# Optimization experiments

Measured on AMD Instinct MI355X. Metric: run time of the kernel, lower is better.

Reference implementation:

```python
import jax, jax.numpy as jnp
import numpy as np

BATCH = 4
STATE_LEN = 8
SEQ_LEN = 4080          # middle tokens; total = SEQ_LEN + 2*STATE_LEN = 4096 (multiple of 8 -> no pad branch)
DIM_IN = 512
DIM_K = 64
DIM_V = 64
SCALE = 0.125           # 1/sqrt(DIM_K)
TOTAL = SEQ_LEN + 2 * STATE_LEN


def setup_inputs() -> dict:
    key = jax.random.key(0)
    ks = jax.random.split(key, 7)
    sd = 1.0 / np.sqrt(DIM_IN)  # ~ nn.Linear init scale
    x = jax.random.normal(ks[0], (BATCH, TOTAL, DIM_IN), dtype=jnp.float32)
    # weights stored as (in, out): y = x @ W  (equivalent to torch Linear with W.T)
    Wq = jax.random.normal(ks[1], (DIM_IN, DIM_K), dtype=jnp.float32) * sd
    Wk = jax.random.normal(ks[2], (DIM_IN, DIM_K), dtype=jnp.float32) * sd
    Wv = jax.random.normal(ks[3], (DIM_IN, DIM_V), dtype=jnp.float32) * sd
    Wq_s = jax.random.normal(ks[4], (DIM_IN, DIM_K), dtype=jnp.float32) * sd
    Wk_s = jax.random.normal(ks[5], (DIM_IN, DIM_K), dtype=jnp.float32) * sd
    Wv_s = jax.random.normal(ks[6], (DIM_IN, DIM_V), dtype=jnp.float32) * sd
    return {"x": x, "Wq": Wq, "Wk": Wk, "Wv": Wv, "Wq_s": Wq_s, "Wk_s": Wk_s, "Wv_s": Wv_s}


def reference(x, Wq, Wk, Wv, Wq_s, Wk_s, Wv_s):
    # extract_state: [state_start | middle | state_end]
    x_ss = x[:, :STATE_LEN]
    x_mid = x[:, STATE_LEN:STATE_LEN + SEQ_LEN]
    x_se = x[:, STATE_LEN + SEQ_LEN:]
    # state tokens use the *_state projections; middle tokens the normal ones
    q = jnp.concatenate([x_ss @ Wq_s, x_mid @ Wq, x_se @ Wq_s], axis=1).astype(jnp.float32)
    k = jnp.concatenate([x_ss @ Wk_s, x_mid @ Wk, x_se @ Wk_s], axis=1).astype(jnp.float32)
    v = jnp.concatenate([x_ss @ Wv_s, x_mid @ Wv, x_se @ Wv_s], axis=1).astype(jnp.float32)
    T = q.shape[1]  # TOTAL
    # scores: (B, T, T); causal mask = log(tril(ones)) == 0 / -inf
    scores = jnp.einsum('bqd,bkd->bqk', q, k) * SCALE
    causal = jnp.tril(jnp.ones((T, T), dtype=bool))
    scores = jnp.where(causal[None], scores, -jnp.inf)
    att = jax.nn.softmax(scores, axis=-1)
    out = jnp.einsum('bqk,bkv->bqv', att, v)
    return out.astype(x.dtype)
```

## Files before the change

kernel.cpp:

```cpp
#include <hip/hip_runtime.h>
#include <hip/hip_bf16.h>

typedef unsigned short u16;
typedef __attribute__((ext_vector_type(8))) short short8;
typedef __attribute__((ext_vector_type(16))) float f32x16;

#define MFMA(A,B,C) __builtin_amdgcn_mfma_f32_32x32x16_bf16(A,B,C,0,0,0)
#define NEG_INF -1e30f

__device__ __forceinline__ unsigned cvtpk_bf16(float a, float b) {
    unsigned r;
    asm("v_cvt_pk_bf16_f32 %0, %1, %2" : "=v"(r) : "v"(a), "v"(b));
    return r;
}
__device__ __forceinline__ void permswap(unsigned &a, unsigned &b) {
    auto r = __builtin_amdgcn_permlane32_swap(a, b, false, false);
    a = r[0]; b = r[1];
}
union W4u { unsigned u[4]; short8 v; };
__device__ __forceinline__ short8 mk8(unsigned a, unsigned b, unsigned c, unsigned d) {
    W4u w; w.u[0] = a; w.u[1] = b; w.u[2] = c; w.u[3] = d; return w.v;
}
__device__ __forceinline__ void split_words(float p0, float p1, unsigned &wh, unsigned &wl) {
    wh = cvtpk_bf16(p0, p1);
    float h0 = __uint_as_float(wh << 16);
    float h1 = __uint_as_float(wh & 0xffff0000u);
    wl = cvtpk_bf16(p0 - h0, p1 - h1);
}
__device__ __forceinline__ void split_store(float v, u16* ph, u16* pl) {
    __hip_bfloat16 h = __float2bfloat16(v);
    float hf = __bfloat162float(h);
    __hip_bfloat16 l = __float2bfloat16(v - hf);
    *ph = *(u16*)&h;
    *pl = *(u16*)&l;
}
__device__ __forceinline__ short8 ld8(const u16* p) { return *(const short8*)p; }

__device__ __forceinline__ int cb64(int qs, int lc) {
    int u = qs >> lc, r = qs - (u << lc);
    return (((u * (u + 1)) >> 1) << lc) + r * (u + 1);
}

__device__ __forceinline__ size_t qk_idx(int grow, int col) {
    return (size_t)(grow >> 5) * 2048 + (col >> 4) * 512 + (grow & 31) * 16
         + ((col >> 3) & 1) * 8 + (col & 7);
}

__device__ __forceinline__ void pack_strip(const f32x16 &ca, const f32x16 &cb,
                                           short8 *pbh, short8 *pbl) {
    unsigned wAh, wAl, wBh, wBl, wCh, wCl, wDh, wDl;
    split_words(ca[0], ca[1], wAh, wAl);   split_words(ca[2], ca[3], wBh, wBl);
    split_words(ca[4], ca[5], wCh, wCl);   split_words(ca[6], ca[7], wDh, wDl);
    permswap(wAh, wCh); permswap(wBh, wDh); permswap(wAl, wCl); permswap(wBl, wDl);
    pbh[0] = mk8(wAh, wBh, wCh, wDh); pbl[0] = mk8(wAl, wBl, wCl, wDl);
    split_words(ca[8], ca[9], wAh, wAl);   split_words(ca[10], ca[11], wBh, wBl);
    split_words(ca[12], ca[13], wCh, wCl); split_words(ca[14], ca[15], wDh, wDl);
    permswap(wAh, wCh); permswap(wBh, wDh); permswap(wAl, wCl); permswap(wBl, wDl);
    pbh[1] = mk8(wAh, wBh, wCh, wDh); pbl[1] = mk8(wAl, wBl, wCl, wDl);
    split_words(cb[0], cb[1], wAh, wAl);   split_words(cb[2], cb[3], wBh, wBl);
    split_words(cb[4], cb[5], wCh, wCl);   split_words(cb[6], cb[7], wDh, wDl);
    permswap(wAh, wCh); permswap(wBh, wDh); permswap(wAl, wCl); permswap(wBl, wDl);
    pbh[2] = mk8(wAh, wBh, wCh, wDh); pbl[2] = mk8(wAl, wBl, wCl, wDl);
    split_words(cb[8], cb[9], wAh, wAl);   split_words(cb[10], cb[11], wBh, wBl);
    split_words(cb[12], cb[13], wCh, wCl); split_words(cb[14], cb[15], wDh, wDl);
    permswap(wAh, wCh); permswap(wBh, wDh); permswap(wAl, wCl); permswap(wBl, wDl);
    pbh[3] = mk8(wAh, wBh, wCh, wDh); pbl[3] = mk8(wAl, wBl, wCl, wDl);
}

__global__ void convw_kernel(
    const float* __restrict__ Wq, const float* __restrict__ Wk, const float* __restrict__ Wv,
    const float* __restrict__ Wqs, const float* __restrict__ Wks, const float* __restrict__ Wvs,
    u16* __restrict__ wbase)
{
    const int z = blockIdx.y;
    const int tile = blockIdx.x;
    const float* W = (z == 0) ? Wq : (z == 1) ? Wk : (z == 2) ? Wv
                   : (z == 3) ? Wqs : (z == 4) ? Wks : Wvs;
    u16* oh = wbase + (size_t)z * 65536;
    u16* ol = oh + 32768;
    __shared__ float Xs[64][65];
    __shared__ u16 stg[8192];
    const int tid = threadIdx.x;
    const int d0 = tile * 64;
    #pragma unroll
    for (int k = 0; k < 16; ++k) {
        int idx = tid + k * 256;
        int d = idx >> 6, c = idx & 63;
        Xs[d][c] = W[(size_t)(d0 + d) * 64 + c];
    }
    __syncthreads();
    #pragma unroll
    for (int k = 0; k < 16; ++k) {
        int odx = tid + k * 256;
        int j = odx & 7, hi8 = (odx >> 3) & 1, r = (odx >> 4) & 63, sl = odx >> 10;
        split_store(Xs[sl * 16 + hi8 * 8 + j][r], &stg[odx], &stg[4096 + odx]);
    }
    __syncthreads();
    #pragma unroll
    for (int rep = 0; rep < 2; ++rep) {
        int i = (tid * 2 + rep) * 8;
        *(short8*)&oh[(size_t)tile * 4096 + i] = *(const short8*)&stg[i];
        *(short8*)&ol[(size_t)tile * 4096 + i] = *(const short8*)&stg[4096 + i];
    }
}

__global__ __launch_bounds__(128, 2) void proj_kernel(
    const float* __restrict__ x, const u16* __restrict__ wbase,
    u16* __restrict__ qh, u16* __restrict__ ql,
    u16* __restrict__ kh, u16* __restrict__ kl,
    u16* __restrict__ vth, u16* __restrict__ vtl)
{
    __shared__ __align__(16) char smraw[24576];
    float (*red)[16][64] = (float (*)[16][64])smraw;
    u16* stg = (u16*)smraw;

    const int bid = blockIdx.x;
    const bool edge = (bid >= 512);
    int sidx;
    if (!edge) { int xcd = bid & 7; sidx = (xcd >> 1) * 128 + (xcd & 1) * 64 + (bid >> 3); }
    else sidx = bid;
    const int w = threadIdx.x >> 6;
    const int lane = threadIdx.x & 63;
    const int l31 = lane & 31, hi = lane >> 5;

    const u16* wb = wbase + (edge ? (size_t)3 * 65536 : 0);
    const u16* wqh_ = wb;                 const u16* wql_ = wb + 32768;
    const u16* wkh_ = wb + 65536;         const u16* wkl_ = wb + 65536 + 32768;
    const u16* wvh_ = wb + 2 * 65536;     const u16* wvl_ = wb + 2 * 65536 + 32768;

    int growA;
    if (!edge) growA = sidx * 32 + l31;
    else {
        int e = sidx - 512, rb = l31 >> 4, i = l31 & 15;
        growA = (2 * e + rb) * 4096 + (i < 8 ? i : 4080 + i);
    }
    const float* xrow = x + (size_t)growA * 512;

    f32x16 aq[2] = {{}, {}}, ak[2] = {{}, {}}, av[2] = {{}, {}};
    const int s0 = w * 16;
    #pragma unroll 2
    for (int si = 0; si < 16; ++si) {
        const int s = s0 + si;
        const int d0 = s * 16 + 8 * hi;
        float4 xa = *(const float4*)(xrow + d0);
        float4 xb = *(const float4*)(xrow + d0 + 4);
        unsigned xh_[4], xl_[4];
        split_words(xa.x, xa.y, xh_[0], xl_[0]);
        split_words(xa.z, xa.w, xh_[1], xl_[1]);
        split_words(xb.x, xb.y, xh_[2], xl_[2]);
        split_words(xb.z, xb.w, xh_[3], xl_[3]);
        short8 xhf = mk8(xh_[0], xh_[1], xh_[2], xh_[3]);
        short8 xlf = mk8(xl_[0], xl_[1], xl_[2], xl_[3]);
        #pragma unroll
        for (int half = 0; half < 2; ++half) {
            size_t wof = (size_t)s * 1024 + (half * 32 + l31) * 16 + hi * 8;
            short8 qH = ld8(wqh_ + wof), qL = ld8(wql_ + wof);
            short8 kH = ld8(wkh_ + wof), kL = ld8(wkl_ + wof);
            short8 vH = ld8(wvh_ + wof), vL = ld8(wvl_ + wof);
            aq[half] = MFMA(xhf, qH, aq[half]);
            aq[half] = MFMA(xhf, qL, aq[half]);
            aq[half] = MFMA(xlf, qH, aq[half]);
            ak[half] = MFMA(xhf, kH, ak[half]);
            ak[half] = MFMA(xhf, kL, ak[half]);
            ak[half] = MFMA(xlf, kH, ak[half]);
            av[half] = MFMA(vH, xhf, av[half]);
            av[half] = MFMA(vL, xhf, av[half]);
            av[half] = MFMA(vH, xlf, av[half]);
        }
    }
    if (w == 1) {
        #pragma unroll
        for (int h = 0; h < 2; ++h)
            #pragma unroll
            for (int r = 0; r < 16; ++r) {
                red[h][r][lane] = aq[h][r];
                red[2 + h][r][lane] = ak[h][r];
            }
    } else {
        #pragma unroll
        for (int h = 0; h < 2; ++h)
            #pragma unroll
            for (int r = 0; r < 16; ++r) red[4 + h][r][lane] = av[h][r];
    }
    __syncthreads();
    if (w == 0) {
        #pragma unroll
        for (int h = 0; h < 2; ++h)
            #pragma unroll
            for (int r = 0; r < 16; ++r) {
                aq[h][r] += red[h][r][lane];
                ak[h][r] += red[2 + h][r][lane];
            }
    } else {
        #pragma unroll
        for (int h = 0; h < 2; ++h)
            #pragma unroll
            for (int r = 0; r < 16; ++r) av[h][r] += red[4 + h][r][lane];
    }
    __syncthreads();

    if (!edge) {
        if (w == 0) {
            #pragma unroll
            for (int half = 0; half < 2; ++half)
                #pragma unroll
                for (int r = 0; r < 16; ++r) {
                    const int crow = (r & 3) + 8 * (r >> 2) + 4 * hi;
                    const int col = half * 32 + l31;
                    int loff = (col >> 4) * 512 + crow * 16 + ((col >> 3) & 1) * 8 + (col & 7);
                    split_store(aq[half][r] * 0.125f, &stg[loff], &stg[2048 + loff]);
                    split_store(ak[half][r], &stg[4096 + loff], &stg[6144 + loff]);
                }
        } else {
            #pragma unroll
            for (int half = 0; half < 2; ++half)
                #pragma unroll
                for (int r = 0; r < 16; ++r) {
                    const int crow = (r & 3) + 8 * (r >> 2) + 4 * hi;
                    int lv = half * 1024 + (l31 >> 4) * 512 + crow * 16
                           + ((l31 >> 3) & 1) * 8 + (l31 & 7);
                    split_store(av[half][r], &stg[8192 + lv], &stg[10240 + lv]);
                }
        }
        __syncthreads();
        const int t128 = threadIdx.x;
        const int sloc = sidx & 127;
        u16* qk0 = qh + (size_t)sidx * 2048;
        u16* qk1 = ql + (size_t)sidx * 2048;
        u16* qk2 = kh + (size_t)sidx * 2048;
        u16* qk3 = kl + (size_t)sidx * 2048;
        #pragma unroll
        for (int rep = 0; rep < 2; ++rep) {
            int i = (t128 * 2 + rep) * 8;
            int crow_ = (i >> 4) & 31;
            int tin = sloc * 32 + crow_;
            if (tin >= 8 && tin < 4088) {
                *(short8*)&qk0[i] = *(const short8*)&stg[i];
                *(short8*)&qk1[i] = *(const short8*)&stg[2048 + i];
                *(short8*)&qk2[i] = *(const short8*)&stg[4096 + i];
                *(short8*)&qk3[i] = *(const short8*)&stg[6144 + i];
            }
        }
        const size_t Vbase = (size_t)(sidx >> 1) * 4096;
        #pragma unroll
        for (int rep = 0; rep < 2; ++rep) {
            int i = (t128 * 2 + rep) * 8;
            int T = ((i >> 9) & 1) * 16 + ((i >> 3) & 1) * 8;
            int tbase = sloc * 32 + T;
            if (tbase >= 8 && tbase < 4088) {
                size_t go = Vbase + (size_t)(i >> 10) * 2048
                          + (((sidx & 1) << 1) + ((i >> 9) & 1)) * 512 + (i & 511);
                *(short8*)&vth[go] = *(const short8*)&stg[8192 + i];
                *(short8*)&vtl[go] = *(const short8*)&stg[10240 + i];
            }
        }
    } else {
        const int bv = growA >> 12, tv = growA & 4095;
        if (w == 0) {
            #pragma unroll
            for (int half = 0; half < 2; ++half)
                #pragma unroll
                for (int r = 0; r < 16; ++r) {
                    const int crow = (r & 3) + 8 * (r >> 2) + 4 * hi;
                    const int col = half * 32 + l31;
                    int e = sidx - 512, rb = crow >> 4, i = crow & 15;
                    int growC = (2 * e + rb) * 4096 + (i < 8 ? i : 4080 + i);
                    size_t qo = qk_idx(growC, col);
                    split_store(aq[half][r] * 0.125f, qh + qo, ql + qo);
                    split_store(ak[half][r], kh + qo, kl + qo);
                }
        } else {
            #pragma unroll
            for (int half = 0; half < 2; ++half)
                #pragma unroll
                for (int r = 0; r < 16; ++r) {
                    const int crow = (r & 3) + 8 * (r >> 2) + 4 * hi;
                    size_t vo = (size_t)(bv * 64 + (tv >> 6)) * 4096 + half * 2048
                              + ((tv & 63) >> 4) * 512 + crow * 16
                              + ((tv >> 3) & 1) * 8 + (tv & 7);
                    split_store(av[half][r], vth + vo, vtl + vo);
                }
        }
    }
}

__global__ __launch_bounds__(64, 2) void flash_kernel(
    const u16* __restrict__ qhB, const u16* __restrict__ qlB,
    const u16* __restrict__ khB, const u16* __restrict__ klB,
    const u16* __restrict__ vthB, const u16* __restrict__ vtlB,
    float* __restrict__ Opart, float* __restrict__ mpart, float* __restrict__ lpart,
    int lc, int G)
{
    const int bid = blockIdx.x;
    const int xcd = bid & 7;
    const int b = xcd >> 1, par = xcd & 1;
    const int rr = bid >> 3;
    const int chunk = (G - 1) - (2 * rr + par);
    int qs = 0;
    for (int step = 32; step; step >>= 1) {
        int cand = qs + step;
        if (cand < 64 && cb64(cand, lc) <= chunk) qs = cand;
    }
    const int cloc = chunk - cb64(qs, lc);
    const int nt = qs + 1;
    const int klo = cloc << lc;
    const int lim = klo + (1 << lc);
    const int khi = (nt < lim) ? nt : lim;
    const int lane = threadIdx.x, l31 = lane & 31, hi = lane >> 5;
    const size_t lane_off = (size_t)(l31 * 16 + hi * 8);

    const size_t qb0 = (size_t)(b * 128 + qs * 2) * 2048 + lane_off;
    short8 q0h[4], q0l[4], q1h[4], q1l[4];
    #pragma unroll
    for (int s = 0; s < 4; ++s) {
        q0h[s] = ld8(qhB + qb0 + s * 512);
        q0l[s] = ld8(qlB + qb0 + s * 512);
        q1h[s] = ld8(qhB + qb0 + 2048 + s * 512);
        q1l[s] = ld8(qlB + qb0 + 2048 + s * 512);
    }

    f32x16 o00 = {}, o01 = {}, o10 = {}, o11 = {};
    float m0 = NEG_INF, l0 = 0.f, m1 = NEG_INF, l1 = 0.f;

    for (int kb = klo; kb < khi; ++kb) {
        const bool diag = (kb == qs);
        const size_t kt = (size_t)(b * 128 + kb * 2) * 2048 + lane_off;
        short8 kf[4];
        f32x16 c00 = {}, c01 = {}, c11 = {};
        f32x16 c10;
        #pragma unroll
        for (int r = 0; r < 16; ++r) c10[r] = diag ? NEG_INF : 0.f;

        #pragma unroll
        for (int s = 0; s < 4; ++s) kf[s] = ld8(khB + kt + s * 512);
        __builtin_amdgcn_s_setprio(1);
        #pragma unroll
        for (int s = 0; s < 4; ++s) {
            c00 = MFMA(kf[s], q0h[s], c00);
            c00 = MFMA(kf[s], q0l[s], c00);
            c01 = MFMA(kf[s], q1h[s], c01);
            c01 = MFMA(kf[s], q1l[s], c01);
        }
        __builtin_amdgcn_s_setprio(0);
        #pragma unroll
        for (int s = 0; s < 4; ++s) kf[s] = ld8(klB + kt + s * 512);
        __builtin_amdgcn_s_setprio(1);
        #pragma unroll
        for (int s = 0; s < 4; ++s) {
            c00 = MFMA(kf[s], q0h[s], c00);
            c01 = MFMA(kf[s], q1h[s], c01);
        }
        __builtin_amdgcn_s_setprio(0);
        #pragma unroll
        for (int s = 0; s < 4; ++s) kf[s] = ld8(khB + kt + 2048 + s * 512);
        __builtin_amdgcn_s_setprio(1);
        if (!diag) {
            #pragma unroll
            for (int s = 0; s < 4; ++s) {
                c10 = MFMA(kf[s], q0h[s], c10);
                c10 = MFMA(kf[s], q0l[s], c10);
            }
        }
        #pragma unroll
        for (int s = 0; s < 4; ++s) {
            c11 = MFMA(kf[s], q1h[s], c11);
            c11 = MFMA(kf[s], q1l[s], c11);
        }
        __builtin_amdgcn_s_setprio(0);
        #pragma unroll
        for (int s = 0; s < 4; ++s) kf[s] = ld8(klB + kt + 2048 + s * 512);
        __builtin_amdgcn_s_setprio(1);
        if (!diag) {
            #pragma unroll
            for (int s = 0; s < 4; ++s) c10 = MFMA(kf[s], q0h[s], c10);
        }
        #pragma unroll
        for (int s = 0; s < 4; ++s) c11 = MFMA(kf[s], q1h[s], c11);
        __builtin_amdgcn_s_setprio(0);

        if (diag) {
            #pragma unroll
            for (int r = 0; r < 16; ++r) {
                int krow = (r & 3) + 8 * (r >> 2) + 4 * hi;
                if (krow > l31) { c00[r] = NEG_INF; c11[r] = NEG_INF; }
            }
        }
        float mx0 = NEG_INF, mx1 = NEG_INF;
        #pragma unroll
        for (int r = 0; r < 16; ++r) {
            mx0 = fmaxf(mx0, fmaxf(c00[r], c10[r]));
            mx1 = fmaxf(mx1, fmaxf(c01[r], c11[r]));
        }
        mx0 = fmaxf(mx0, __shfl_xor(mx0, 32));
        mx1 = fmaxf(mx1, __shfl_xor(mx1, 32));
        float mn0 = fmaxf(m0, mx0), mn1 = fmaxf(m1, mx1);
        float al0 = __expf(m0 - mn0), al1 = __expf(m1 - mn1);
        m0 = mn0; m1 = mn1;
        float s0 = 0.f, s1 = 0.f;
        #pragma unroll
        for (int r = 0; r < 16; ++r) {
            c00[r] = __expf(c00[r] - mn0); s0 += c00[r];
            c10[r] = __expf(c10[r] - mn0); s0 += c10[r];
            c01[r] = __expf(c01[r] - mn1); s1 += c01[r];
            c11[r] = __expf(c11[r] - mn1); s1 += c11[r];
        }
        s0 += __shfl_xor(s0, 32);
        s1 += __shfl_xor(s1, 32);
        l0 = l0 * al0 + s0;
        l1 = l1 * al1 + s1;
        #pragma unroll
        for (int r = 0; r < 16; ++r) {
            o00[r] *= al0; o10[r] *= al0;
            o01[r] *= al1; o11[r] *= al1;
        }
        short8 p0h[4], p0l[4], p1h[4], p1l[4];
        pack_strip(c00, c10, p0h, p0l);
        pack_strip(c01, c11, p1h, p1l);

        __builtin_amdgcn_sched_barrier(0);
        const size_t vt = (size_t)(b * 64 + kb) * 4096 + lane_off;
        short8 vh_[4], vl_[4];
        #pragma unroll
        for (int s = 0; s < 4; ++s) {
            vh_[s] = ld8(vthB + vt + s * 512);
            vl_[s] = ld8(vtlB + vt + s * 512);
        }
        __builtin_amdgcn_s_setprio(1);
        #pragma unroll
        for (int s = 0; s < 4; ++s) {
            o00 = MFMA(vh_[s], p0h[s], o00);
            o00 = MFMA(vh_[s], p0l[s], o00);
            o00 = MFMA(vl_[s], p0h[s], o00);
            o01 = MFMA(vh_[s], p1h[s], o01);
            o01 = MFMA(vh_[s], p1l[s], o01);
            o01 = MFMA(vl_[s], p1h[s], o01);
        }
        __builtin_amdgcn_s_setprio(0);
        #pragma unroll
        for (int s = 0; s < 4; ++s) {
            vh_[s] = ld8(vthB + vt + 2048 + s * 512);
            vl_[s] = ld8(vtlB + vt + 2048 + s * 512);
        }
        __builtin_amdgcn_s_setprio(1);
        #pragma unroll
        for (int s = 0; s < 4; ++s) {
            o10 = MFMA(vh_[s], p0h[s], o10);
            o10 = MFMA(vh_[s], p0l[s], o10);
            o10 = MFMA(vl_[s], p0h[s], o10);
            o11 = MFMA(vh_[s], p1h[s], o11);
            o11 = MFMA(vh_[s], p1l[s], o11);
            o11 = MFMA(vl_[s], p1h[s], o11);
        }
        __builtin_amdgcn_s_setprio(0);
    }
    const int pid = b * G + chunk;
    float* Op = Opart + (size_t)pid * 4096;
    #pragma unroll
    for (int r = 0; r < 16; ++r) {
        int v0 = (r & 3) + 8 * (r >> 2) + 4 * hi;
        Op[v0 * 64 + l31]        = o00[r];
        Op[v0 * 64 + 32 + l31]   = o01[r];
        Op[(v0 + 32) * 64 + l31]      = o10[r];
        Op[(v0 + 32) * 64 + 32 + l31] = o11[r];
    }
    if (hi == 0) {
        mpart[pid * 64 + l31] = m0;       lpart[pid * 64 + l31] = l0;
        mpart[pid * 64 + 32 + l31] = m1;  lpart[pid * 64 + 32 + l31] = l1;
    }
}

__global__ void merge_kernel(
    const float* __restrict__ Opart, const float* __restrict__ mpart,
    const float* __restrict__ lpart, float* __restrict__ out, int lc, int G)
{
    __shared__ float wgt[32][64];
    __shared__ float tr[64][65];
    const int bid = blockIdx.x;
    const int b = bid >> 6, qs = bid & 63;
    const int g = (qs + (1 << lc)) >> lc;
    const int base = b * G + cb64(qs, lc);
    const int tid = threadIdx.x;
    if (tid < 64) {
        float M = NEG_INF;
        for (int s = 0; s < g; ++s) M = fmaxf(M, mpart[(base + s) * 64 + tid]);
        float L = 0.f;
        for (int s = 0; s < g; ++s)
            L += lpart[(base + s) * 64 + tid] * __expf(mpart[(base + s) * 64 + tid] - M);
        float inv = 1.0f / L;
        for (int s = 0; s < g; ++s)
            wgt[s][tid] = __expf(mpart[(base + s) * 64 + tid] - M) * inv;
    }
    __syncthreads();
    float acc[16] = {};
    for (int s = 0; s < g; ++s) {
        const float* Op = Opart + (size_t)(base + s) * 4096;
        #pragma unroll
        for (int k = 0; k < 16; ++k) {
            int i = tid + k * 256;
            acc[k] += wgt[s][i & 63] * Op[i];
        }
    }
    #pragma unroll
    for (int k = 0; k < 16; ++k) {
        int i = tid + k * 256;
        tr[i & 63][i >> 6] = acc[k];
    }
    __syncthreads();
    float* dst = out + ((size_t)b * 4096 + qs * 64) * 64;
    #pragma unroll
    for (int k = 0; k < 16; ++k) {
        int j = tid + k * 256;
        dst[j] = tr[j >> 6][j & 63];
    }
}

extern "C" void kernel_launch(void* const* d_in, const int* in_sizes, int n_in,
                              void* d_out, int out_size, void* d_ws, size_t ws_size,
                              hipStream_t stream) {
    const float* x   = (const float*)d_in[0];
    const float* Wq  = (const float*)d_in[1];
    const float* Wk  = (const float*)d_in[2];
    const float* Wv  = (const float*)d_in[3];
    const float* Wqs = (const float*)d_in[4];
    const float* Wks = (const float*)d_in[5];
    const float* Wvs = (const float*)d_in[6];
    float* out = (float*)d_out;

    char* ws = (char*)d_ws;
    const size_t MB = 1024 * 1024;
    u16* qh  = (u16*)(ws);
    u16* ql  = (u16*)(ws + 2 * MB);
    u16* kh  = (u16*)(ws + 4 * MB);
    u16* kl  = (u16*)(ws + 6 * MB);
    u16* vth = (u16*)(ws + 8 * MB);
    u16* vtl = (u16*)(ws + 10 * MB);
    u16* wbase = (u16*)(ws + 12 * MB);
    float* mpart = (float*)(ws + 13 * MB);
    float* lpart = (float*)(ws + 14 * MB + 512 * 1024);
    float* Opart = (float*)(ws + 16 * MB);

    int LC = 1, G = 1056;
    if (ws_size < 16 * MB + (size_t)4 * 1056 * 16384) { LC = 2; G = 544; }
    if (ws_size < 16 * MB + (size_t)4 * 544  * 16384) { LC = 3; G = 288; }

    convw_kernel<<<dim3(8, 6), 256, 0, stream>>>(Wq, Wk, Wv, Wqs, Wks, Wvs, wbase);
    proj_kernel<<<514, 128, 0, stream>>>(x, wbase, qh, ql, kh, kl, vth, vtl);
    flash_kernel<<<4 * G, 64, 0, stream>>>(qh, ql, kh, kl, vth, vtl,
                                           Opart, mpart, lpart, LC, G);
    merge_kernel<<<256, 256, 0, stream>>>(Opart, mpart, lpart, out, LC, G);
}
```

Baseline: 174.2 us.

## Drop low-bf16 halves of K and V, use exp2 with folded log2e scale

K and V are now stored only as single bf16 (high part), while Q keeps its hi/lo split. This removes the kl/vtl workspace buffers and their loads, and cuts the QK MFMA count from 6 to 4 per strip and the PV count from 3 to 2 per accumulator. The softmax scale now includes log2(e), so a raw v_exp_f32 (exp2) replaces __expf in the flash and merge kernels. The K and V loads are hoisted ahead of the MFMA blocks, and the default split count changes from LC=1 to LC=2. Dropping the K/V low halves lowers accuracy, roughly to bf16 precision on K and V.

```diff
diff --git a/kernel.cpp b/kernel.cpp
--- a/kernel.cpp
+++ b/kernel.cpp
@@ -7,7 +7,13 @@
 
 #define MFMA(A,B,C) __builtin_amdgcn_mfma_f32_32x32x16_bf16(A,B,C,0,0,0)
 #define NEG_INF -1e30f
-
+#define QSC (0.125f * 1.44269504f)
+
+__device__ __forceinline__ float exp2_fast(float x) {
+    float r;
+    asm("v_exp_f32 %0, %1" : "=v"(r) : "v"(x));
+    return r;
+}
 __device__ __forceinline__ unsigned cvtpk_bf16(float a, float b) {
     unsigned r;
     asm("v_cvt_pk_bf16_f32 %0, %1, %2" : "=v"(r) : "v"(a), "v"(b));
@@ -33,6 +39,10 @@
     __hip_bfloat16 l = __float2bfloat16(v - hf);
     *ph = *(u16*)&h;
     *pl = *(u16*)&l;
+}
+__device__ __forceinline__ void store_hi(float v, u16* ph) {
+    __hip_bfloat16 h = __float2bfloat16(v);
+    *ph = *(u16*)&h;
 }
 __device__ __forceinline__ short8 ld8(const u16* p) { return *(const short8*)p; }
 
@@ -107,8 +117,7 @@
 __global__ __launch_bounds__(128, 2) void proj_kernel(
     const float* __restrict__ x, const u16* __restrict__ wbase,
     u16* __restrict__ qh, u16* __restrict__ ql,
-    u16* __restrict__ kh, u16* __restrict__ kl,
-    u16* __restrict__ vth, u16* __restrict__ vtl)
+    u16* __restrict__ kh, u16* __restrict__ vth)
 {
     __shared__ __align__(16) char smraw[24576];
     float (*red)[16][64] = (float (*)[16][64])smraw;
@@ -208,8 +217,8 @@
                     const int crow = (r & 3) + 8 * (r >> 2) + 4 * hi;
                     const int col = half * 32 + l31;
                     int loff = (col >> 4) * 512 + crow * 16 + ((col >> 3) & 1) * 8 + (col & 7);
-                    split_store(aq[half][r] * 0.125f, &stg[loff], &stg[2048 + loff]);
-                    split_store(ak[half][r], &stg[4096 + loff], &stg[6144 + loff]);
+                    split_store(aq[half][r] * QSC, &stg[loff], &stg[2048 + loff]);
+                    store_hi(ak[half][r], &stg[4096 + loff]);
                 }
         } else {
             #pragma unroll
@@ -219,7 +228,7 @@
                     const int crow = (r & 3) + 8 * (r >> 2) + 4 * hi;
                     int lv = half * 1024 + (l31 >> 4) * 512 + crow * 16
                            + ((l31 >> 3) & 1) * 8 + (l31 & 7);
-                    split_store(av[half][r], &stg[8192 + lv], &stg[10240 + lv]);
+                    store_hi(av[half][r], &stg[6144 + lv]);
                 }
         }
         __syncthreads();
@@ -228,7 +237,6 @@
         u16* qk0 = qh + (size_t)sidx * 2048;
         u16* qk1 = ql + (size_t)sidx * 2048;
         u16* qk2 = kh + (size_t)sidx * 2048;
-        u16* qk3 = kl + (size_t)sidx * 2048;
         #pragma unroll
         for (int rep = 0; rep < 2; ++rep) {
             int i = (t128 * 2 + rep) * 8;
@@ -238,7 +246,6 @@
                 *(short8*)&qk0[i] = *(const short8*)&stg[i];
                 *(short8*)&qk1[i] = *(const short8*)&stg[2048 + i];
                 *(short8*)&qk2[i] = *(const short8*)&stg[4096 + i];
-                *(short8*)&qk3[i] = *(const short8*)&stg[6144 + i];
             }
         }
         const size_t Vbase = (size_t)(sidx >> 1) * 4096;
@@ -250,8 +257,7 @@
             if (tbase >= 8 && tbase < 4088) {
                 size_t go = Vbase + (size_t)(i >> 10) * 2048
                           + (((sidx & 1) << 1) + ((i >> 9) & 1)) * 512 + (i & 511);
-                *(short8*)&vth[go] = *(const short8*)&stg[8192 + i];
-                *(short8*)&vtl[go] = *(const short8*)&stg[10240 + i];
+                *(short8*)&vth[go] = *(const short8*)&stg[6144 + i];
             }
         }
     } else {
@@ -266,8 +272,8 @@
                     int e = sidx - 512, rb = crow >> 4, i = crow & 15;
                     int growC = (2 * e + rb) * 4096 + (i < 8 ? i : 4080 + i);
                     size_t qo = qk_idx(growC, col);
-                    split_store(aq[half][r] * 0.125f, qh + qo, ql + qo);
-                    split_store(ak[half][r], kh + qo, kl + qo);
+                    split_store(aq[half][r] * QSC, qh + qo, ql + qo);
+                    store_hi(ak[half][r], kh + qo);
                 }
         } else {
             #pragma unroll
@@ -278,7 +284,7 @@
                     size_t vo = (size_t)(bv * 64 + (tv >> 6)) * 4096 + half * 2048
                               + ((tv & 63) >> 4) * 512 + crow * 16
                               + ((tv >> 3) & 1) * 8 + (tv & 7);
-                    split_store(av[half][r], vth + vo, vtl + vo);
+                    store_hi(av[half][r], vth + vo);
                 }
         }
     }
@@ -286,8 +292,7 @@
 
 __global__ __launch_bounds__(64, 2) void flash_kernel(
     const u16* __restrict__ qhB, const u16* __restrict__ qlB,
-    const u16* __restrict__ khB, const u16* __restrict__ klB,
-    const u16* __restrict__ vthB, const u16* __restrict__ vtlB,
+    const u16* __restrict__ khB, const u16* __restrict__ vthB,
     float* __restrict__ Opart, float* __restrict__ mpart, float* __restrict__ lpart,
     int lc, int G)
 {
@@ -325,58 +330,46 @@
     for (int kb = klo; kb < khi; ++kb) {
         const bool diag = (kb == qs);
         const size_t kt = (size_t)(b * 128 + kb * 2) * 2048 + lane_off;
-        short8 kf[4];
+        short8 kf0[4], kf1[4];
+        #pragma unroll
+        for (int s = 0; s < 4; ++s) {
+            kf0[s] = ld8(khB + kt + s * 512);
+            kf1[s] = ld8(khB + kt + 2048 + s * 512);
+        }
         f32x16 c00 = {}, c01 = {}, c11 = {};
         f32x16 c10;
         #pragma unroll
         for (int r = 0; r < 16; ++r) c10[r] = diag ? NEG_INF : 0.f;
 
-        #pragma unroll
-        for (int s = 0; s < 4; ++s) kf[s] = ld8(khB + kt + s * 512);
         __builtin_amdgcn_s_setprio(1);
         #pragma unroll
         for (int s = 0; s < 4; ++s) {
-            c00 = MFMA(kf[s], q0h[s], c00);
-            c00 = MFMA(kf[s], q0l[s], c00);
-            c01 = MFMA(kf[s], q1h[s], c01);
-            c01 = MFMA(kf[s], q1l[s], c01);
+            c00 = MFMA(kf0[s], q0h[s], c00);
+            c00 = MFMA(kf0[s], q0l[s], c00);
+            c01 = MFMA(kf0[s], q1h[s], c01);
+            c01 = MFMA(kf0[s], q1l[s], c01);
+        }
+        if (!diag) {
+            #pragma unroll
+            for (int s = 0; s < 4; ++s) {
+                c10 = MFMA(kf1[s], q0h[s], c10);
+                c10 = MFMA(kf1[s], q0l[s], c10);
+            }
+        }
+        #pragma unroll
+        for (int s = 0; s < 4; ++s) {
+            c11 = MFMA(kf1[s], q1h[s], c11);
+            c11 = MFMA(kf1[s], q1l[s], c11);
         }
         __builtin_amdgcn_s_setprio(0);
-        #pragma unroll
-        for (int s = 0; s < 4; ++s) kf[s] = ld8(klB + kt + s * 512);
-        __builtin_amdgcn_s_setprio(1);
+
+        const size_t vt = (size_t)(b * 64 + kb) * 4096 + lane_off;
+        short8 v0[4], v1[4];
         #pragma unroll
         for (int s = 0; s < 4; ++s) {
-            c00 = MFMA(kf[s], q0h[s], c00);
-            c01 = MFMA(kf[s], q1h[s], c01);
-        }
-        __builtin_amdgcn_s_setprio(0);
-        #pragma unroll
-        for (int s = 0; s < 4; ++s) kf[s] = ld8(khB + kt + 2048 + s * 512);
-        __builtin_amdgcn_s_setprio(1);
-        if (!diag) {
-            #pragma unroll
-            for (int s = 0; s < 4; ++s) {
-                c10 = MFMA(kf[s], q0h[s], c10);
-                c10 = MFMA(kf[s], q0l[s], c10);
-            }
-        }
-        #pragma unroll
-        for (int s = 0; s < 4; ++s) {
-            c11 = MFMA(kf[s], q1h[s], c11);
-            c11 = MFMA(kf[s], q1l[s], c11);
-        }
-        __builtin_amdgcn_s_setprio(0);
-        #pragma unroll
-        for (int s = 0; s < 4; ++s) kf[s] = ld8(klB + kt + 2048 + s * 512);
-        __builtin_amdgcn_s_setprio(1);
-        if (!diag) {
-            #pragma unroll
-            for (int s = 0; s < 4; ++s) c10 = MFMA(kf[s], q0h[s], c10);
-        }
-        #pragma unroll
-        for (int s = 0; s < 4; ++s) c11 = MFMA(kf[s], q1h[s], c11);
-        __builtin_amdgcn_s_setprio(0);
+            v0[s] = ld8(vthB + vt + s * 512);
+            v1[s] = ld8(vthB + vt + 2048 + s * 512);
+        }
 
         if (diag) {
             #pragma unroll
@@ -394,15 +387,15 @@
         mx0 = fmaxf(mx0, __shfl_xor(mx0, 32));
         mx1 = fmaxf(mx1, __shfl_xor(mx1, 32));
         float mn0 = fmaxf(m0, mx0), mn1 = fmaxf(m1, mx1);
-        float al0 = __expf(m0 - mn0), al1 = __expf(m1 - mn1);
+        float al0 = exp2_fast(m0 - mn0), al1 = exp2_fast(m1 - mn1);
         m0 = mn0; m1 = mn1;
         float s0 = 0.f, s1 = 0.f;
         #pragma unroll
         for (int r = 0; r < 16; ++r) {
-            c00[r] = __expf(c00[r] - mn0); s0 += c00[r];
-            c10[r] = __expf(c10[r] - mn0); s0 += c10[r];
-            c01[r] = __expf(c01[r] - mn1); s1 += c01[r];
-            c11[r] = __expf(c11[r] - mn1); s1 += c11[r];
+            c00[r] = exp2_fast(c00[r] - mn0); s0 += c00[r];
+            c10[r] = exp2_fast(c10[r] - mn0); s0 += c10[r];
+            c01[r] = exp2_fast(c01[r] - mn1); s1 += c01[r];
+            c11[r] = exp2_fast(c11[r] - mn1); s1 += c11[r];
         }
         s0 += __shfl_xor(s0, 32);
         s1 += __shfl_xor(s1, 32);
@@ -417,39 +410,17 @@
         pack_strip(c00, c10, p0h, p0l);
         pack_strip(c01, c11, p1h, p1l);
 
-        __builtin_amdgcn_sched_barrier(0);
-        const size_t vt = (size_t)(b * 64 + kb) * 4096 + lane_off;
-        short8 vh_[4], vl_[4];
+        __builtin_amdgcn_s_setprio(1);
         #pragma unroll
         for (int s = 0; s < 4; ++s) {
-            vh_[s] = ld8(vthB + vt + s * 512);
-            vl_[s] = ld8(vtlB + vt + s * 512);
-        }
-        __builtin_amdgcn_s_setprio(1);
-        #pragma unroll
-        for (int s = 0; s < 4; ++s) {
-            o00 = MFMA(vh_[s], p0h[s], o00);
-            o00 = MFMA(vh_[s], p0l[s], o00);
-            o00 = MFMA(vl_[s], p0h[s], o00);
-            o01 = MFMA(vh_[s], p1h[s], o01);
-            o01 = MFMA(vh_[s], p1l[s], o01);
-            o01 = MFMA(vl_[s], p1h[s], o01);
-        }
-        __builtin_amdgcn_s_setprio(0);
-        #pragma unroll
-        for (int s = 0; s < 4; ++s) {
-            vh_[s] = ld8(vthB + vt + 2048 + s * 512);
-            vl_[s] = ld8(vtlB + vt + 2048 + s * 512);
-        }
-        __builtin_amdgcn_s_setprio(1);
-        #pragma unroll
-        for (int s = 0; s < 4; ++s) {
-            o10 = MFMA(vh_[s], p0h[s], o10);
-            o10 = MFMA(vh_[s], p0l[s], o10);
-            o10 = MFMA(vl_[s], p0h[s], o10);
-            o11 = MFMA(vh_[s], p1h[s], o11);
-            o11 = MFMA(vh_[s], p1l[s], o11);
-            o11 = MFMA(vl_[s], p1h[s], o11);
+            o00 = MFMA(v0[s], p0h[s], o00);
+            o00 = MFMA(v0[s], p0l[s], o00);
+            o01 = MFMA(v0[s], p1h[s], o01);
+            o01 = MFMA(v0[s], p1l[s], o01);
+            o10 = MFMA(v1[s], p0h[s], o10);
+            o10 = MFMA(v1[s], p0l[s], o10);
+            o11 = MFMA(v1[s], p1h[s], o11);
+            o11 = MFMA(v1[s], p1l[s], o11);
         }
         __builtin_amdgcn_s_setprio(0);
     }
@@ -457,11 +428,11 @@
     float* Op = Opart + (size_t)pid * 4096;
     #pragma unroll
     for (int r = 0; r < 16; ++r) {
-        int v0 = (r & 3) + 8 * (r >> 2) + 4 * hi;
-        Op[v0 * 64 + l31]        = o00[r];
-        Op[v0 * 64 + 32 + l31]   = o01[r];
-        Op[(v0 + 32) * 64 + l31]      = o10[r];
-        Op[(v0 + 32) * 64 + 32 + l31] = o11[r];
+        int v0i = (r & 3) + 8 * (r >> 2) + 4 * hi;
+        Op[v0i * 64 + l31]             = o00[r];
+        Op[v0i * 64 + 32 + l31]        = o01[r];
+        Op[(v0i + 32) * 64 + l31]      = o10[r];
+        Op[(v0i + 32) * 64 + 32 + l31] = o11[r];
     }
     if (hi == 0) {
         mpart[pid * 64 + l31] = m0;       lpart[pid * 64 + l31] = l0;
@@ -485,10 +456,10 @@
         for (int s = 0; s < g; ++s) M = fmaxf(M, mpart[(base + s) * 64 + tid]);
         float L = 0.f;
         for (int s = 0; s < g; ++s)
-            L += lpart[(base + s) * 64 + tid] * __expf(mpart[(base + s) * 64 + tid] - M);
+            L += lpart[(base + s) * 64 + tid] * exp2_fast(mpart[(base + s) * 64 + tid] - M);
         float inv = 1.0f / L;
         for (int s = 0; s < g; ++s)
-            wgt[s][tid] = __expf(mpart[(base + s) * 64 + tid] - M) * inv;
+            wgt[s][tid] = exp2_fast(mpart[(base + s) * 64 + tid] - M) * inv;
     }
     __syncthreads();
     float acc[16] = {};
@@ -531,21 +502,19 @@
     u16* qh  = (u16*)(ws);
     u16* ql  = (u16*)(ws + 2 * MB);
     u16* kh  = (u16*)(ws + 4 * MB);
-    u16* kl  = (u16*)(ws + 6 * MB);
-    u16* vth = (u16*)(ws + 8 * MB);
-    u16* vtl = (u16*)(ws + 10 * MB);
-    u16* wbase = (u16*)(ws + 12 * MB);
-    float* mpart = (float*)(ws + 13 * MB);
-    float* lpart = (float*)(ws + 14 * MB + 512 * 1024);
-    float* Opart = (float*)(ws + 16 * MB);
-
-    int LC = 1, G = 1056;
-    if (ws_size < 16 * MB + (size_t)4 * 1056 * 16384) { LC = 2; G = 544; }
-    if (ws_size < 16 * MB + (size_t)4 * 544  * 16384) { LC = 3; G = 288; }
+    u16* vth = (u16*)(ws + 6 * MB);
+    u16* wbase = (u16*)(ws + 8 * MB);
+    float* mpart = (float*)(ws + 9 * MB);
+    float* lpart = (float*)(ws + 10 * MB);
+    float* Opart = (float*)(ws + 11 * MB);
+
+    int LC = 2, G = 544;
+    if (ws_size < 11 * MB + (size_t)4 * 544 * 16384) { LC = 3; G = 288; }
+    if (ws_size < 11 * MB + (size_t)4 * 288 * 16384) { LC = 4; G = 160; }
 
     convw_kernel<<<dim3(8, 6), 256, 0, stream>>>(Wq, Wk, Wv, Wqs, Wks, Wvs, wbase);
-    proj_kernel<<<514, 128, 0, stream>>>(x, wbase, qh, ql, kh, kl, vth, vtl);
-    flash_kernel<<<4 * G, 64, 0, stream>>>(qh, ql, kh, kl, vth, vtl,
+    proj_kernel<<<514, 128, 0, stream>>>(x, wbase, qh, ql, kh, vth);
+    flash_kernel<<<4 * G, 64, 0, stream>>>(qh, ql, kh, vth,
                                            Opart, mpart, lpart, LC, G);
     merge_kernel<<<256, 256, 0, stream>>>(Opart, mpart, lpart, out, LC, G);
 }
```

New measurement: 160.6 us. 7.8% less time.
